# Performance work log

Hardware: AMD Instinct MI355X
Metric: run time of the kernel (lower is better)

The kernel has to match this reference:

```python
import jax, jax.numpy as jnp
import numpy as np

N_NODES = 100000
N_EDGES = 1600000
D = 64  # latent = hidden = output = 64


def gcn_conv(x, W, b, src, dst, n):
    # PyG GCNConv: out = D^{-1/2} (A + I) D^{-1/2} (x W) + b, self-loops added.
    h = x @ W  # [N, d_out]
    ones = jnp.ones(src.shape[0], dtype=h.dtype)
    deg = jax.ops.segment_sum(ones, dst, num_segments=n) + 1.0  # +1 for self-loop
    dinv = jax.lax.rsqrt(deg)  # [N]
    norm = dinv[src] * dinv[dst]  # [E]
    msgs = h[src] * norm[:, None]  # gather + scale, [E, d_out]
    agg = jax.ops.segment_sum(msgs, dst, num_segments=n)  # scatter-add
    # self-loop contribution: dinv[i]^2 * h[i]
    agg = agg + h * (dinv * dinv)[:, None]
    return agg + b


def setup_inputs() -> dict:
    key = jax.random.key(0)
    ks = jax.random.split(key, 9)
    s = 1.0 / np.sqrt(D)
    return {
        "z": jax.random.normal(ks[0], (N_NODES, D), dtype=jnp.float32),
        "src": jax.random.randint(ks[1], (N_EDGES,), 0, N_NODES, dtype=jnp.int32),
        "dst": jax.random.randint(ks[2], (N_EDGES,), 0, N_NODES, dtype=jnp.int32),
        "W1": jax.random.uniform(ks[3], (D, D), jnp.float32, -s, s),
        "b1": jnp.zeros((D,), jnp.float32),
        "W2": jax.random.uniform(ks[4], (D, D), jnp.float32, -s, s),
        "b2": jnp.zeros((D,), jnp.float32),
        "W3": jax.random.uniform(ks[5], (D, D), jnp.float32, -s, s),
        "b3": jnp.zeros((D,), jnp.float32),
    }


def reference(z, src, dst, W1, b1, W2, b2, W3, b3):
    n = z.shape[0]
    x = jax.nn.relu(gcn_conv(z, W1, b1, src, dst, n))
    x = jax.nn.relu(gcn_conv(x, W2, b2, src, dst, n))
    x = gcn_conv(x, W3, b3, src, dst, n)
    return x
```

## Files before the change

### kernel.cpp

```cpp
#include <hip/hip_runtime.h>
#include <hip/hip_fp16.h>

#define N_NODES 100000
#define N_EDGES 1600000
#define N_BUCKETS 512
#define BUCKET_NODES 196
#define BKT_BLOCKS 512
#define CAP_E 4096
#define CAP_C 6144
#define DUMMY N_NODES

typedef unsigned short u16;
typedef _Float16 f16x8 __attribute__((ext_vector_type(8)));
typedef float f32x4 __attribute__((ext_vector_type(4)));
typedef unsigned u32x4 __attribute__((ext_vector_type(4)));

__device__ __forceinline__ u16 f2h(float f) {
    return __half_as_ushort(__float2half_rn(f));
}

__device__ __forceinline__ u32x4 gload16(const char* addr) {
    u32x4 d;
    asm volatile("global_load_dwordx4 %0, %1, off" : "=v"(d) : "v"(addr));
    return d;
}

__device__ __forceinline__ void acc8v(float* acc, u32x4 q) {
#pragma unroll
    for (int i = 0; i < 4; ++i) {
        unsigned w = q[i];
        __half2 h = *reinterpret_cast<__half2*>(&w);
        float2 f = __half22float2(h);
        acc[2 * i] += f.x;
        acc[2 * i + 1] += f.y;
    }
}

__device__ __forceinline__ void acc8(float* acc, uint4 q) {
    unsigned v[4] = {q.x, q.y, q.z, q.w};
#pragma unroll
    for (int i = 0; i < 4; ++i) {
        __half2 h = *reinterpret_cast<__half2*>(&v[i]);
        float2 f = __half22float2(h);
        acc[2 * i] += f.x;
        acc[2 * i + 1] += f.y;
    }
}

__global__ __launch_bounds__(256) void k_bucket(const int* __restrict__ src,
                                                const int* __restrict__ dst,
                                                int* __restrict__ btot,
                                                int* __restrict__ ebuf,
                                                const float* __restrict__ W1,
                                                const float* __restrict__ W2,
                                                const float* __restrict__ W3,
                                                u16* __restrict__ Wp) {
    __shared__ int cnt[N_BUCKETS], base_s[N_BUCKETS];
    if (blockIdx.x >= BKT_BLOCKS) {
        int wb = blockIdx.x - BKT_BLOCKS;
        const float* W = wb == 0 ? W1 : (wb == 1 ? W2 : W3);
        u16* o = Wp + wb * 4096;
        for (int f = threadIdx.x; f < 4096; f += 256) {
            int j = f & 7, l16 = (f >> 3) & 15, quad = (f >> 7) & 3;
            int c = (f >> 9) & 1, t = f >> 10;
            o[f] = f2h(W[(quad * 8 + 32 * c + j) * 64 + 4 * l16 + t]);
        }
        return;
    }
    const int CS = N_EDGES / BKT_BLOCKS;
    int t = threadIdx.x;
    int beg = blockIdx.x * CS, end = beg + CS;
    for (int i = t; i < N_BUCKETS; i += 256) cnt[i] = 0;
    __syncthreads();
    for (int e = beg + t; e < end; e += 256)
        atomicAdd(&cnt[(unsigned)dst[e] / BUCKET_NODES], 1);
    __syncthreads();
    for (int i = t; i < N_BUCKETS; i += 256) {
        base_s[i] = atomicAdd(&btot[i], cnt[i]);
        cnt[i] = 0;
    }
    __syncthreads();
    for (int e = beg + t; e < end; e += 256) {
        int d = dst[e], s = src[e];
        int b = (unsigned)d / BUCKET_NODES;
        int l = atomicAdd(&cnt[b], 1);
        ebuf[b * CAP_E + base_s[b] + l] = s | ((d - b * BUCKET_NODES) << 17);
    }
}

__global__ __launch_bounds__(512) void k_build(const int* __restrict__ btot,
                                               const int* __restrict__ ebuf,
                                               int* __restrict__ col,
                                               int2* __restrict__ rowinfo,
                                               float* __restrict__ dinv,
                                               const float* __restrict__ z,
                                               u16* __restrict__ xs,
                                               u16* __restrict__ xs_other) {
    __shared__ int deg[BUCKET_NODES];
    __shared__ int cur[BUCKET_NODES];
    __shared__ int wsum[4];
    __shared__ int cls[CAP_C];
    int b = blockIdx.x, t = threadIdx.x;
    int nb = b * BUCKET_NODES;
    int nn = N_NODES - nb;
    if (nn > BUCKET_NODES) nn = BUCKET_NODES;
    int ne = btot[b];
    const int* eb = ebuf + b * CAP_E;

    for (int i = t; i < BUCKET_NODES; i += 512) deg[i] = 0;
    __syncthreads();
    for (int e = t; e < ne; e += 512) atomicAdd(&deg[eb[e] >> 17], 1);
    __syncthreads();

    int pv = (t < nn) ? ((deg[t] + 7) & ~7) : 0;
    int v = pv;
    int lane = t & 63, wv = t >> 6;
#pragma unroll
    for (int off = 1; off < 64; off <<= 1) {
        int u = __shfl_up(v, off, 64);
        if (lane >= off) v += u;
    }
    if (t < 256 && lane == 63) wsum[wv] = v;
    __syncthreads();
    int total = wsum[0] + wsum[1] + wsum[2] + wsum[3];
    int add = 0;
    for (int i = 0; i < wv && i < 4; ++i) add += wsum[i];
    int incl = v + add;

    int colbase = b * CAP_C;
    if (t < nn) {
        int off0 = incl - pv;
        cur[t] = off0;
        rowinfo[nb + t] = make_int2(colbase + off0, pv);
        dinv[nb + t] = rsqrtf((float)deg[t] + 1.0f);
    }
    __syncthreads();
    for (int i = t; i < total; i += 512) cls[i] = DUMMY << 7;
    __syncthreads();
    for (int e = t; e < ne; e += 512) {
        int pe = eb[e];
        int l = atomicAdd(&cur[pe >> 17], 1);
        cls[l] = (pe & 0x1FFFF) << 7;
    }
    __syncthreads();
    for (int i = t; i < total; i += 512) col[colbase + i] = cls[i];
    if (t < 16) col[colbase + total + t] = DUMMY << 7;

    const float4* zz = (const float4*)(z + (size_t)nb * 64);
    uint2* xx = (uint2*)(xs + (size_t)nb * 64);
    for (int i = t; i < nn * 16; i += 512) {
        float4 vv = zz[i];
        float dd = rsqrtf((float)deg[i >> 4] + 1.0f);
        unsigned p0 = (unsigned)f2h(vv.x * dd) | ((unsigned)f2h(vv.y * dd) << 16);
        unsigned p1 = (unsigned)f2h(vv.z * dd) | ((unsigned)f2h(vv.w * dd) << 16);
        xx[i] = make_uint2(p0, p1);
    }
    if (b == 0 && t < 8) {
        ((uint4*)(xs + (size_t)N_NODES * 64))[t] = make_uint4(0, 0, 0, 0);
        ((uint4*)(xs_other + (size_t)N_NODES * 64))[t] = make_uint4(0, 0, 0, 0);
    }
}

__global__ __launch_bounds__(256, 3) void k_agg(const int2* __restrict__ rowinfo,
                                                const int* __restrict__ col,
                                                const float* __restrict__ dinv,
                                                const u16* __restrict__ xs,
                                                u16* __restrict__ h) {
    const int lane = threadIdx.x & 63;
    const int eighth = lane >> 3;
    const int fh = lane & 7;
    const char* xb = (const char*)xs;
    int wave = (blockIdx.x * blockDim.x + threadIdx.x) >> 6;
    int nwaves = (gridDim.x * blockDim.x) >> 6;

    for (int n0 = wave * 4; n0 < N_NODES; n0 += nwaves * 4) {
        int u0 = __builtin_amdgcn_readfirstlane(n0);
        int2 r0 = rowinfo[u0];
        int2 r1 = rowinfo[u0 + 1];
        int2 r2 = rowinfo[u0 + 2];
        int2 r3 = rowinfo[u0 + 3];
        int it0 = r0.y >> 4, it1 = r1.y >> 4, it2 = r2.y >> 4, it3 = r3.y >> 4;
        int itm = it0 > it1 ? it0 : it1;
        if (it2 > itm) itm = it2;
        if (it3 > itm) itm = it3;

        int2 c0 = *(const int2*)(col + r0.x + 2 * eighth);
        int2 c1 = *(const int2*)(col + r1.x + 2 * eighth);
        int2 c2 = *(const int2*)(col + r2.x + 2 * eighth);
        int2 c3 = *(const int2*)(col + r3.x + 2 * eighth);
        int tc0 = col[r0.x + (it0 << 4) + eighth];
        int tc1 = col[r1.x + (it1 << 4) + eighth];
        int tc2 = col[r2.x + (it2 << 4) + eighth];
        int tc3 = col[r3.x + (it3 << 4) + eighth];
        float d0 = dinv[u0];
        float d1 = dinv[u0 + 1];
        float d2 = dinv[u0 + 2];
        float d3 = dinv[u0 + 3];

        u32x4 q0 = gload16(xb + (unsigned)c0.x + fh * 16);
        u32x4 q1 = gload16(xb + (unsigned)c0.y + fh * 16);
        u32x4 q2 = gload16(xb + (unsigned)c1.x + fh * 16);
        u32x4 q3 = gload16(xb + (unsigned)c1.y + fh * 16);
        u32x4 q4 = gload16(xb + (unsigned)c2.x + fh * 16);
        u32x4 q5 = gload16(xb + (unsigned)c2.y + fh * 16);
        u32x4 q6 = gload16(xb + (unsigned)c3.x + fh * 16);
        u32x4 q7 = gload16(xb + (unsigned)c3.y + fh * 16);
        u32x4 g0 = gload16(xb + (unsigned)tc0 + fh * 16);
        u32x4 g1 = gload16(xb + (unsigned)tc1 + fh * 16);
        u32x4 g2 = gload16(xb + (unsigned)tc2 + fh * 16);
        u32x4 g3 = gload16(xb + (unsigned)tc3 + fh * 16);
        u32x4 s0 = gload16(xb + (size_t)u0 * 128 + fh * 16);
        u32x4 s1 = gload16(xb + (size_t)(u0 + 1) * 128 + fh * 16);
        u32x4 s2 = gload16(xb + (size_t)(u0 + 2) * 128 + fh * 16);
        u32x4 s3 = gload16(xb + (size_t)(u0 + 3) * 128 + fh * 16);
        asm volatile("s_waitcnt vmcnt(0)" ::: "memory");
        __builtin_amdgcn_sched_barrier(0);

        float a0[8] = {0.f, 0.f, 0.f, 0.f, 0.f, 0.f, 0.f, 0.f};
        float a1[8] = {0.f, 0.f, 0.f, 0.f, 0.f, 0.f, 0.f, 0.f};
        float a2[8] = {0.f, 0.f, 0.f, 0.f, 0.f, 0.f, 0.f, 0.f};
        float a3[8] = {0.f, 0.f, 0.f, 0.f, 0.f, 0.f, 0.f, 0.f};
        if (0 < it0) { acc8v(a0, q0); acc8v(a0, q1); }
        if (0 < it1) { acc8v(a1, q2); acc8v(a1, q3); }
        if (0 < it2) { acc8v(a2, q4); acc8v(a2, q5); }
        if (0 < it3) { acc8v(a3, q6); acc8v(a3, q7); }
        if ((r0.y >> 3) & 1) acc8v(a0, g0);
        if ((r1.y >> 3) & 1) acc8v(a1, g1);
        if ((r2.y >> 3) & 1) acc8v(a2, g2);
        if ((r3.y >> 3) & 1) acc8v(a3, g3);
        if (eighth == 0) acc8v(a0, s0);
        if (eighth == 1) acc8v(a1, s1);
        if (eighth == 2) acc8v(a2, s2);
        if (eighth == 3) acc8v(a3, s3);

        for (int rr = 1; rr < itm; ++rr) {
            int2 e0 = *(const int2*)(col + r0.x + ((rr < it0 ? rr : 0) << 4) + 2 * eighth);
            int2 e1 = *(const int2*)(col + r1.x + ((rr < it1 ? rr : 0) << 4) + 2 * eighth);
            int2 e2 = *(const int2*)(col + r2.x + ((rr < it2 ? rr : 0) << 4) + 2 * eighth);
            int2 e3 = *(const int2*)(col + r3.x + ((rr < it3 ? rr : 0) << 4) + 2 * eighth);
            uint4 p0 = *(const uint4*)(xb + (unsigned)e0.x + fh * 16);
            uint4 p1 = *(const uint4*)(xb + (unsigned)e0.y + fh * 16);
            uint4 p2 = *(const uint4*)(xb + (unsigned)e1.x + fh * 16);
            uint4 p3 = *(const uint4*)(xb + (unsigned)e1.y + fh * 16);
            uint4 p4 = *(const uint4*)(xb + (unsigned)e2.x + fh * 16);
            uint4 p5 = *(const uint4*)(xb + (unsigned)e2.y + fh * 16);
            uint4 p6 = *(const uint4*)(xb + (unsigned)e3.x + fh * 16);
            uint4 p7 = *(const uint4*)(xb + (unsigned)e3.y + fh * 16);
            if (rr < it0) { acc8(a0, p0); acc8(a0, p1); }
            if (rr < it1) { acc8(a1, p2); acc8(a1, p3); }
            if (rr < it2) { acc8(a2, p4); acc8(a2, p5); }
            if (rr < it3) { acc8(a3, p6); acc8(a3, p7); }
        }

#pragma unroll
        for (int m = 8; m <= 32; m <<= 1) {
#pragma unroll
            for (int j = 0; j < 8; ++j) {
                a0[j] += __shfl_xor(a0[j], m, 64);
                a1[j] += __shfl_xor(a1[j], m, 64);
                a2[j] += __shfl_xor(a2[j], m, 64);
                a3[j] += __shfl_xor(a3[j], m, 64);
            }
        }
        uint4 p0, p1, p2, p3;
        u16* pp0 = (u16*)&p0;
        u16* pp1 = (u16*)&p1;
        u16* pp2 = (u16*)&p2;
        u16* pp3 = (u16*)&p3;
#pragma unroll
        for (int j = 0; j < 8; ++j) {
            pp0[j] = f2h(a0[j] * d0);
            pp1[j] = f2h(a1[j] * d1);
            pp2[j] = f2h(a2[j] * d2);
            pp3[j] = f2h(a3[j] * d3);
        }
        if (eighth == 0) ((uint4*)(h + (size_t)u0 * 64))[fh] = p0;
        if (eighth == 1) ((uint4*)(h + (size_t)(u0 + 1) * 64))[fh] = p1;
        if (eighth == 2) ((uint4*)(h + (size_t)(u0 + 2) * 64))[fh] = p2;
        if (eighth == 3) ((uint4*)(h + (size_t)(u0 + 3) * 64))[fh] = p3;
    }
}

__global__ __launch_bounds__(256) void k_mv(const u16* __restrict__ h,
                                            const u16* __restrict__ Wp,
                                            const float* __restrict__ bias,
                                            const float* __restrict__ dinv,
                                            u16* __restrict__ outh,
                                            float* __restrict__ outf, int hidden) {
    const int lane = threadIdx.x & 63;
    const int quad = lane >> 4;
    const int l16 = lane & 15;

    const uint4* wq = (const uint4*)Wp;
    union { uint4 u; f16x8 f; } bfr[4][2];
#pragma unroll
    for (int t = 0; t < 4; ++t)
#pragma unroll
        for (int c = 0; c < 2; ++c)
            bfr[t][c].u = wq[t * 128 + c * 64 + quad * 16 + l16];
    float4 bq = ((const float4*)bias)[l16];
    float bv[4] = {bq.x, bq.y, bq.z, bq.w};

    int wave = (blockIdx.x * blockDim.x + threadIdx.x) >> 6;
    int nwaves = (gridDim.x * blockDim.x) >> 6;
    for (int chunk = wave; chunk < N_NODES / 16; chunk += nwaves) {
        int row0 = chunk * 16;
        const u16* hb = h + (size_t)row0 * 64;
        union { uint4 u; f16x8 f; } a0, a1;
        a0.u = *(const uint4*)(hb + l16 * 64 + quad * 8);
        a1.u = *(const uint4*)(hb + l16 * 64 + quad * 8 + 32);

        f32x4 acc[4] = {{0.f, 0.f, 0.f, 0.f}, {0.f, 0.f, 0.f, 0.f},
                        {0.f, 0.f, 0.f, 0.f}, {0.f, 0.f, 0.f, 0.f}};
#pragma unroll
        for (int t = 0; t < 4; ++t) {
            acc[t] = __builtin_amdgcn_mfma_f32_16x16x32_f16(a0.f, bfr[t][0].f, acc[t], 0, 0, 0);
            acc[t] = __builtin_amdgcn_mfma_f32_16x16x32_f16(a1.f, bfr[t][1].f, acc[t], 0, 0, 0);
        }
        float dv[4];
#pragma unroll
        for (int r = 0; r < 4; ++r) dv[r] = dinv[row0 + quad * 4 + r];
#pragma unroll
        for (int r = 0; r < 4; ++r) {
            int row = row0 + quad * 4 + r;
            float o[4];
#pragma unroll
            for (int t = 0; t < 4; ++t) o[t] = acc[t][r] + bv[t];
            if (hidden) {
                float dd = dv[r];
#pragma unroll
                for (int t = 0; t < 4; ++t) o[t] = fmaxf(o[t], 0.f) * dd;
                unsigned lo = (unsigned)f2h(o[0]) | ((unsigned)f2h(o[1]) << 16);
                unsigned hi = (unsigned)f2h(o[2]) | ((unsigned)f2h(o[3]) << 16);
                ((uint2*)(outh + (size_t)row * 64))[l16] = make_uint2(lo, hi);
            } else {
                ((float4*)(outf + (size_t)row * 64))[l16] =
                    make_float4(o[0], o[1], o[2], o[3]);
            }
        }
    }
}

extern "C" void kernel_launch(void* const* d_in, const int* in_sizes, int n_in,
                              void* d_out, int out_size, void* d_ws, size_t ws_size,
                              hipStream_t stream) {
    const float* z  = (const float*)d_in[0];
    const int* src  = (const int*)d_in[1];
    const int* dst  = (const int*)d_in[2];
    const float* W1 = (const float*)d_in[3];
    const float* b1 = (const float*)d_in[4];
    const float* W2 = (const float*)d_in[5];
    const float* b2 = (const float*)d_in[6];
    const float* W3 = (const float*)d_in[7];
    const float* b3 = (const float*)d_in[8];
    float* out = (float*)d_out;

    char* p = (char*)d_ws;
    float* dinv    = (float*)p;  p += (size_t)512 << 10;
    int2*  rowinfo = (int2*)p;   p += (size_t)1 << 20;
    int*   btot    = (int*)p;    p += (size_t)4 << 10;
    int*   ebuf    = (int*)p;    p += (size_t)N_BUCKETS * CAP_E * 4;
    int*   col     = (int*)p;    p += (size_t)N_BUCKETS * CAP_C * 4;
    u16*   hbuf    = (u16*)p;    p += (size_t)13 << 20;
    u16*   buf0    = (u16*)p;    p += (size_t)13 << 20;
    u16*   buf1    = (u16*)p;    p += (size_t)13 << 20;
    u16*   wp      = (u16*)p;

    const int gA = 6250;
    const int gM = 1563;

    hipMemsetAsync(btot, 0, N_BUCKETS * sizeof(int), stream);
    k_bucket<<<BKT_BLOCKS + 3, 256, 0, stream>>>(src, dst, btot, ebuf, W1, W2, W3, wp);
    k_build<<<N_BUCKETS, 512, 0, stream>>>(btot, ebuf, col, rowinfo, dinv, z, buf0, buf1);

    k_agg<<<gA, 256, 0, stream>>>(rowinfo, col, dinv, buf0, hbuf);
    k_mv <<<gM, 256, 0, stream>>>(hbuf, wp, b1, dinv, buf1, nullptr, 1);
    k_agg<<<gA, 256, 0, stream>>>(rowinfo, col, dinv, buf1, hbuf);
    k_mv <<<gM, 256, 0, stream>>>(hbuf, wp + 4096, b2, dinv, buf0, nullptr, 1);
    k_agg<<<gA, 256, 0, stream>>>(rowinfo, col, dinv, buf0, hbuf);
    k_mv <<<gM, 256, 0, stream>>>(hbuf, wp + 8192, b3, dinv, nullptr, out, 0);
}
```

Baseline: 257.0 us.

## Split feature matrix into four column chunks to shrink the gather working set per pass

Stores node features as four 16-column fp16 chunks (32 bytes per node per chunk) and launches aggregation over a 2D grid, one chunk per grid y. Each chunk's working set is a quarter of the full feature matrix, so random neighbor gathers are meant to hit in cache more often. Each wave now handles two nodes with 32 lanes per node. Col indices are read with nontemporal loads and the explicit batched-prefetch asm is dropped. The trade-off is that column indices are re-read four times, the gathers are only 16 bytes wide, and there is less memory-level parallelism per wave.

```diff
diff --git a/kernel.cpp b/kernel.cpp
--- a/kernel.cpp
+++ b/kernel.cpp
@@ -9,31 +9,15 @@
 #define CAP_E 4096
 #define CAP_C 6144
 #define DUMMY N_NODES
+#define NCHUNK 4
+#define CHUNKB 3276800
 
 typedef unsigned short u16;
 typedef _Float16 f16x8 __attribute__((ext_vector_type(8)));
 typedef float f32x4 __attribute__((ext_vector_type(4)));
-typedef unsigned u32x4 __attribute__((ext_vector_type(4)));
 
 __device__ __forceinline__ u16 f2h(float f) {
     return __half_as_ushort(__float2half_rn(f));
-}
-
-__device__ __forceinline__ u32x4 gload16(const char* addr) {
-    u32x4 d;
-    asm volatile("global_load_dwordx4 %0, %1, off" : "=v"(d) : "v"(addr));
-    return d;
-}
-
-__device__ __forceinline__ void acc8v(float* acc, u32x4 q) {
-#pragma unroll
-    for (int i = 0; i < 4; ++i) {
-        unsigned w = q[i];
-        __half2 h = *reinterpret_cast<__half2*>(&w);
-        float2 f = __half22float2(h);
-        acc[2 * i] += f.x;
-        acc[2 * i + 1] += f.y;
-    }
 }
 
 __device__ __forceinline__ void acc8(float* acc, uint4 q) {
@@ -135,150 +119,88 @@
         dinv[nb + t] = rsqrtf((float)deg[t] + 1.0f);
     }
     __syncthreads();
-    for (int i = t; i < total; i += 512) cls[i] = DUMMY << 7;
+    for (int i = t; i < total; i += 512) cls[i] = DUMMY << 5;
     __syncthreads();
     for (int e = t; e < ne; e += 512) {
         int pe = eb[e];
         int l = atomicAdd(&cur[pe >> 17], 1);
-        cls[l] = (pe & 0x1FFFF) << 7;
+        cls[l] = (pe & 0x1FFFF) << 5;
     }
     __syncthreads();
     for (int i = t; i < total; i += 512) col[colbase + i] = cls[i];
-    if (t < 16) col[colbase + total + t] = DUMMY << 7;
+    if (t < 16) col[colbase + total + t] = DUMMY << 5;
 
     const float4* zz = (const float4*)(z + (size_t)nb * 64);
-    uint2* xx = (uint2*)(xs + (size_t)nb * 64);
     for (int i = t; i < nn * 16; i += 512) {
+        int nodei = i >> 4, g = i & 15, c = g >> 2, part = g & 3;
         float4 vv = zz[i];
-        float dd = rsqrtf((float)deg[i >> 4] + 1.0f);
+        float dd = rsqrtf((float)deg[nodei] + 1.0f);
         unsigned p0 = (unsigned)f2h(vv.x * dd) | ((unsigned)f2h(vv.y * dd) << 16);
         unsigned p1 = (unsigned)f2h(vv.z * dd) | ((unsigned)f2h(vv.w * dd) << 16);
-        xx[i] = make_uint2(p0, p1);
-    }
-    if (b == 0 && t < 8) {
-        ((uint4*)(xs + (size_t)N_NODES * 64))[t] = make_uint4(0, 0, 0, 0);
-        ((uint4*)(xs_other + (size_t)N_NODES * 64))[t] = make_uint4(0, 0, 0, 0);
-    }
-}
-
-__global__ __launch_bounds__(256, 3) void k_agg(const int2* __restrict__ rowinfo,
-                                                const int* __restrict__ col,
-                                                const float* __restrict__ dinv,
-                                                const u16* __restrict__ xs,
-                                                u16* __restrict__ h) {
+        *(uint2*)((char*)xs + (size_t)c * CHUNKB + (size_t)(nb + nodei) * 32 +
+                  part * 8) = make_uint2(p0, p1);
+    }
+    if (b == 0 && t < 32) {
+        int tt = t & 15, c = tt >> 2, part = tt & 3;
+        char* base = (t < 16) ? (char*)xs : (char*)xs_other;
+        *(uint2*)(base + (size_t)c * CHUNKB + (size_t)DUMMY * 32 + part * 8) =
+            make_uint2(0, 0);
+    }
+}
+
+__global__ __launch_bounds__(256) void k_agg(const int2* __restrict__ rowinfo,
+                                             const int* __restrict__ col,
+                                             const float* __restrict__ dinv,
+                                             const u16* __restrict__ xs,
+                                             u16* __restrict__ h) {
     const int lane = threadIdx.x & 63;
-    const int eighth = lane >> 3;
-    const int fh = lane & 7;
-    const char* xb = (const char*)xs;
+    const int node = lane >> 5;
+    const int slot16 = (lane >> 1) & 15;
+    const int slot8 = (lane >> 1) & 7;
+    const int hb = lane & 1;
+    const char* xc = (const char*)xs + (size_t)blockIdx.y * CHUNKB;
+    char* hc = (char*)h + (size_t)blockIdx.y * CHUNKB;
+
     int wave = (blockIdx.x * blockDim.x + threadIdx.x) >> 6;
-    int nwaves = (gridDim.x * blockDim.x) >> 6;
-
-    for (int n0 = wave * 4; n0 < N_NODES; n0 += nwaves * 4) {
-        int u0 = __builtin_amdgcn_readfirstlane(n0);
-        int2 r0 = rowinfo[u0];
-        int2 r1 = rowinfo[u0 + 1];
-        int2 r2 = rowinfo[u0 + 2];
-        int2 r3 = rowinfo[u0 + 3];
-        int it0 = r0.y >> 4, it1 = r1.y >> 4, it2 = r2.y >> 4, it3 = r3.y >> 4;
-        int itm = it0 > it1 ? it0 : it1;
-        if (it2 > itm) itm = it2;
-        if (it3 > itm) itm = it3;
-
-        int2 c0 = *(const int2*)(col + r0.x + 2 * eighth);
-        int2 c1 = *(const int2*)(col + r1.x + 2 * eighth);
-        int2 c2 = *(const int2*)(col + r2.x + 2 * eighth);
-        int2 c3 = *(const int2*)(col + r3.x + 2 * eighth);
-        int tc0 = col[r0.x + (it0 << 4) + eighth];
-        int tc1 = col[r1.x + (it1 << 4) + eighth];
-        int tc2 = col[r2.x + (it2 << 4) + eighth];
-        int tc3 = col[r3.x + (it3 << 4) + eighth];
-        float d0 = dinv[u0];
-        float d1 = dinv[u0 + 1];
-        float d2 = dinv[u0 + 2];
-        float d3 = dinv[u0 + 3];
-
-        u32x4 q0 = gload16(xb + (unsigned)c0.x + fh * 16);
-        u32x4 q1 = gload16(xb + (unsigned)c0.y + fh * 16);
-        u32x4 q2 = gload16(xb + (unsigned)c1.x + fh * 16);
-        u32x4 q3 = gload16(xb + (unsigned)c1.y + fh * 16);
-        u32x4 q4 = gload16(xb + (unsigned)c2.x + fh * 16);
-        u32x4 q5 = gload16(xb + (unsigned)c2.y + fh * 16);
-        u32x4 q6 = gload16(xb + (unsigned)c3.x + fh * 16);
-        u32x4 q7 = gload16(xb + (unsigned)c3.y + fh * 16);
-        u32x4 g0 = gload16(xb + (unsigned)tc0 + fh * 16);
-        u32x4 g1 = gload16(xb + (unsigned)tc1 + fh * 16);
-        u32x4 g2 = gload16(xb + (unsigned)tc2 + fh * 16);
-        u32x4 g3 = gload16(xb + (unsigned)tc3 + fh * 16);
-        u32x4 s0 = gload16(xb + (size_t)u0 * 128 + fh * 16);
-        u32x4 s1 = gload16(xb + (size_t)(u0 + 1) * 128 + fh * 16);
-        u32x4 s2 = gload16(xb + (size_t)(u0 + 2) * 128 + fh * 16);
-        u32x4 s3 = gload16(xb + (size_t)(u0 + 3) * 128 + fh * 16);
-        asm volatile("s_waitcnt vmcnt(0)" ::: "memory");
-        __builtin_amdgcn_sched_barrier(0);
-
-        float a0[8] = {0.f, 0.f, 0.f, 0.f, 0.f, 0.f, 0.f, 0.f};
-        float a1[8] = {0.f, 0.f, 0.f, 0.f, 0.f, 0.f, 0.f, 0.f};
-        float a2[8] = {0.f, 0.f, 0.f, 0.f, 0.f, 0.f, 0.f, 0.f};
-        float a3[8] = {0.f, 0.f, 0.f, 0.f, 0.f, 0.f, 0.f, 0.f};
-        if (0 < it0) { acc8v(a0, q0); acc8v(a0, q1); }
-        if (0 < it1) { acc8v(a1, q2); acc8v(a1, q3); }
-        if (0 < it2) { acc8v(a2, q4); acc8v(a2, q5); }
-        if (0 < it3) { acc8v(a3, q6); acc8v(a3, q7); }
-        if ((r0.y >> 3) & 1) acc8v(a0, g0);
-        if ((r1.y >> 3) & 1) acc8v(a1, g1);
-        if ((r2.y >> 3) & 1) acc8v(a2, g2);
-        if ((r3.y >> 3) & 1) acc8v(a3, g3);
-        if (eighth == 0) acc8v(a0, s0);
-        if (eighth == 1) acc8v(a1, s1);
-        if (eighth == 2) acc8v(a2, s2);
-        if (eighth == 3) acc8v(a3, s3);
-
-        for (int rr = 1; rr < itm; ++rr) {
-            int2 e0 = *(const int2*)(col + r0.x + ((rr < it0 ? rr : 0) << 4) + 2 * eighth);
-            int2 e1 = *(const int2*)(col + r1.x + ((rr < it1 ? rr : 0) << 4) + 2 * eighth);
-            int2 e2 = *(const int2*)(col + r2.x + ((rr < it2 ? rr : 0) << 4) + 2 * eighth);
-            int2 e3 = *(const int2*)(col + r3.x + ((rr < it3 ? rr : 0) << 4) + 2 * eighth);
-            uint4 p0 = *(const uint4*)(xb + (unsigned)e0.x + fh * 16);
-            uint4 p1 = *(const uint4*)(xb + (unsigned)e0.y + fh * 16);
-            uint4 p2 = *(const uint4*)(xb + (unsigned)e1.x + fh * 16);
-            uint4 p3 = *(const uint4*)(xb + (unsigned)e1.y + fh * 16);
-            uint4 p4 = *(const uint4*)(xb + (unsigned)e2.x + fh * 16);
-            uint4 p5 = *(const uint4*)(xb + (unsigned)e2.y + fh * 16);
-            uint4 p6 = *(const uint4*)(xb + (unsigned)e3.x + fh * 16);
-            uint4 p7 = *(const uint4*)(xb + (unsigned)e3.y + fh * 16);
-            if (rr < it0) { acc8(a0, p0); acc8(a0, p1); }
-            if (rr < it1) { acc8(a1, p2); acc8(a1, p3); }
-            if (rr < it2) { acc8(a2, p4); acc8(a2, p5); }
-            if (rr < it3) { acc8(a3, p6); acc8(a3, p7); }
-        }
-
-#pragma unroll
-        for (int m = 8; m <= 32; m <<= 1) {
-#pragma unroll
-            for (int j = 0; j < 8; ++j) {
-                a0[j] += __shfl_xor(a0[j], m, 64);
-                a1[j] += __shfl_xor(a1[j], m, 64);
-                a2[j] += __shfl_xor(a2[j], m, 64);
-                a3[j] += __shfl_xor(a3[j], m, 64);
-            }
-        }
-        uint4 p0, p1, p2, p3;
-        u16* pp0 = (u16*)&p0;
-        u16* pp1 = (u16*)&p1;
-        u16* pp2 = (u16*)&p2;
-        u16* pp3 = (u16*)&p3;
-#pragma unroll
-        for (int j = 0; j < 8; ++j) {
-            pp0[j] = f2h(a0[j] * d0);
-            pp1[j] = f2h(a1[j] * d1);
-            pp2[j] = f2h(a2[j] * d2);
-            pp3[j] = f2h(a3[j] * d3);
-        }
-        if (eighth == 0) ((uint4*)(h + (size_t)u0 * 64))[fh] = p0;
-        if (eighth == 1) ((uint4*)(h + (size_t)(u0 + 1) * 64))[fh] = p1;
-        if (eighth == 2) ((uint4*)(h + (size_t)(u0 + 2) * 64))[fh] = p2;
-        if (eighth == 3) ((uint4*)(h + (size_t)(u0 + 3) * 64))[fh] = p3;
-    }
+    int u0 = __builtin_amdgcn_readfirstlane(wave * 2);
+    int2 r0 = rowinfo[u0];
+    int2 r1 = rowinfo[u0 + 1];
+    int2 rn = node ? r1 : r0;
+    int itn = rn.y >> 4;
+    int it0 = r0.y >> 4, it1 = r1.y >> 4;
+    int itm = it0 > it1 ? it0 : it1;
+
+    int cm = __builtin_nontemporal_load(col + rn.x + slot16);
+    int tc = __builtin_nontemporal_load(col + rn.x + (itn << 4) + slot8);
+    uint4 q = *(const uint4*)(xc + (unsigned)cm + hb * 16);
+    uint4 g = *(const uint4*)(xc + (unsigned)tc + hb * 16);
+    uint4 s = *(const uint4*)(xc + (size_t)(u0 + node) * 32 + hb * 16);
+    float dv = dinv[u0 + node];
+
+    float a[8] = {0.f, 0.f, 0.f, 0.f, 0.f, 0.f, 0.f, 0.f};
+    if (0 < itn) acc8(a, q);
+    if (((rn.y >> 3) & 1) && !(lane & 16)) acc8(a, g);
+
+    for (int rr = 1; rr < itm; ++rr) {
+        int c2 = __builtin_nontemporal_load(
+            col + rn.x + ((rr < itn ? rr : 0) << 4) + slot16);
+        uint4 q2 = *(const uint4*)(xc + (unsigned)c2 + hb * 16);
+        if (rr < itn) acc8(a, q2);
+    }
+
+#pragma unroll
+    for (int m = 2; m <= 16; m <<= 1) {
+#pragma unroll
+        for (int j = 0; j < 8; ++j) a[j] += __shfl_xor(a[j], m, 64);
+    }
+    acc8(a, s);
+
+    uint4 p;
+    u16* pp = (u16*)&p;
+#pragma unroll
+    for (int j = 0; j < 8; ++j) pp[j] = f2h(a[j] * dv);
+    if (slot16 == 0)
+        *(uint4*)(hc + (size_t)(u0 + node) * 32 + hb * 16) = p;
 }
 
 __global__ __launch_bounds__(256) void k_mv(const u16* __restrict__ h,
@@ -290,6 +212,7 @@
     const int lane = threadIdx.x & 63;
     const int quad = lane >> 4;
     const int l16 = lane & 15;
+    const char* hb8 = (const char*)h;
 
     const uint4* wq = (const uint4*)Wp;
     union { uint4 u; f16x8 f; } bfr[4][2];
@@ -305,10 +228,10 @@
     int nwaves = (gridDim.x * blockDim.x) >> 6;
     for (int chunk = wave; chunk < N_NODES / 16; chunk += nwaves) {
         int row0 = chunk * 16;
-        const u16* hb = h + (size_t)row0 * 64;
         union { uint4 u; f16x8 f; } a0, a1;
-        a0.u = *(const uint4*)(hb + l16 * 64 + quad * 8);
-        a1.u = *(const uint4*)(hb + l16 * 64 + quad * 8 + 32);
+        size_t roff = (size_t)(row0 + l16) * 32 + (quad & 1) * 16;
+        a0.u = *(const uint4*)(hb8 + (size_t)(quad >> 1) * CHUNKB + roff);
+        a1.u = *(const uint4*)(hb8 + (size_t)(2 + (quad >> 1)) * CHUNKB + roff);
 
         f32x4 acc[4] = {{0.f, 0.f, 0.f, 0.f}, {0.f, 0.f, 0.f, 0.f},
                         {0.f, 0.f, 0.f, 0.f}, {0.f, 0.f, 0.f, 0.f}};
@@ -332,7 +255,8 @@
                 for (int t = 0; t < 4; ++t) o[t] = fmaxf(o[t], 0.f) * dd;
                 unsigned lo = (unsigned)f2h(o[0]) | ((unsigned)f2h(o[1]) << 16);
                 unsigned hi = (unsigned)f2h(o[2]) | ((unsigned)f2h(o[3]) << 16);
-                ((uint2*)(outh + (size_t)row * 64))[l16] = make_uint2(lo, hi);
+                *(uint2*)((char*)outh + (size_t)(l16 >> 2) * CHUNKB +
+                          (size_t)row * 32 + (l16 & 3) * 8) = make_uint2(lo, hi);
             } else {
                 ((float4*)(outf + (size_t)row * 64))[l16] =
                     make_float4(o[0], o[1], o[2], o[3]);
@@ -366,7 +290,7 @@
     u16*   buf1    = (u16*)p;    p += (size_t)13 << 20;
     u16*   wp      = (u16*)p;
 
-    const int gA = 6250;
+    const dim3 gA(12500, NCHUNK);
     const int gM = 1563;
 
     hipMemsetAsync(btot, 0, N_BUCKETS * sizeof(int), stream);
```

After: 388.2 us. +51.0%, slower.
